# Performance work log

Measured on AMD Instinct MI355X. Metric: run time of the kernel, lower is better.

## Reference

```python
import jax, jax.numpy as jnp
import numpy as np

B, S, V, H, K, T = 4, 256, 32000, 1024, 4, 20
THRESHOLD = 0.6


def setup_inputs() -> dict:
    key = jax.random.key(0)
    ks = jax.random.split(key, 12)
    sH = 1.0 / np.sqrt(H)
    return {
        "input_ids": jax.random.randint(ks[0], (B, S), 0, V),
        "labels": jax.random.randint(ks[1], (B, S), 0, V),
        "embed": jax.random.normal(ks[2], (V, H), jnp.float32) * 0.02,
        "W1": jax.random.normal(ks[3], (H, H), jnp.float32) * sH,
        "b1": jnp.zeros((H,), jnp.float32),
        "lm_head": jax.random.normal(ks[4], (H, V), jnp.float32) * 0.02,
        "W_gen": jax.random.normal(ks[5], (H, H), jnp.float32) * sH,
        "thought_emb": jax.random.normal(ks[6], (K, H), jnp.float32) * 0.02,
        "tpos_emb": jax.random.normal(ks[7], (T, H), jnp.float32) * 0.02,
        "w_score": jax.random.normal(ks[8], (2 * H,), jnp.float32) * sH,
        "w_gate": jax.random.normal(ks[9], (2 * H,), jnp.float32) * sH,
    }


def reference(input_ids, labels, embed, W1, b1, lm_head, W_gen,
              thought_emb, tpos_emb, w_score, w_gate):
    # ---- base model: embed -> tanh MLP -> lm_head ----
    h0 = embed[input_ids]                                 # (B,S,H)
    hidden = jnp.tanh(h0 @ W1 + b1)                       # base last_hidden_state
    base_logits = hidden @ lm_head                        # (B,S,V)

    # ---- ThoughtInjector: per-position gate from normalized entropy ----
    logp = jax.nn.log_softmax(base_logits, axis=-1)
    ent = -jnp.sum(jnp.exp(logp) * logp, axis=-1) / jnp.log(float(V))  # (B,S)
    inject = (ent.mean(axis=0) > THRESHOLD) & (jnp.arange(S) < S - 1)   # (S,)

    # ---- ThoughtGenerator: (B,S,K,T,H) thoughts (masked dispatch, all pos) ----
    g = jnp.tanh(hidden @ W_gen)                          # (B,S,H)
    thoughts = jnp.tanh(g[:, :, None, None, :]
                        + thought_emb[None, None, :, None, :]
                        + tpos_emb[None, None, None, :, :])  # (B,S,K,T,H)
    tmean = thoughts.mean(axis=3)                         # (B,S,K,H) = thoughts.mean(dim=2)

    # ---- CoherenceScorer: composite score per thought ----
    comp = jax.nn.sigmoid(
        jnp.einsum('bsh,h->bs', hidden, w_score[:H])[:, :, None]
        + jnp.einsum('bskh,h->bsk', tmean, w_score[H:]))  # (B,S,K)

    # ---- MixingHead: coherence-weighted thought mix, gated blend with hidden ----
    alpha = jax.nn.softmax(comp, axis=-1)                 # (B,S,K)
    mixed_thought = jnp.einsum('bsk,bskh->bsh', alpha, tmean)
    gate = jax.nn.sigmoid(jnp.einsum('bsh,h->bs', hidden, w_gate[:H])
                          + jnp.einsum('bsh,h->bs', mixed_thought, w_gate[H:]))[..., None]
    mixed = gate * mixed_thought + (1.0 - gate) * hidden

    enhanced = jnp.where(inject[None, :, None], mixed, hidden)
    final_logits = enhanced @ lm_head                     # (B,S,V)

    # ---- shifted cross-entropy loss ----
    sl = jax.nn.log_softmax(final_logits[:, :-1, :], axis=-1)
    loss = -jnp.take_along_axis(sl, labels[:, 1:, None], axis=-1).mean()
    return final_logits, loss
```

## Files before the change

kernel.cpp:

```cpp
#include <hip/hip_runtime.h>


#define V_SZ 32000
#define H_SZ 1024
#define S_SZ 256
#define B_SZ 4
#define M_SZ 1024
#define K_TH 4
#define T_TH 20
#define NTILE_V 250
#define PARTS (NTILE_V * 2)

typedef __bf16 bf16_t;
typedef __bf16 bf16x8 __attribute__((ext_vector_type(8)));
typedef __bf16 bf16x4 __attribute__((ext_vector_type(4)));
typedef float  f32x4  __attribute__((ext_vector_type(4)));

typedef __attribute__((address_space(1))) void gvoid_t;
typedef __attribute__((address_space(3))) void lvoid_t;

__device__ __forceinline__ void async_copy16(const bf16_t* g, bf16_t* l) {
  __builtin_amdgcn_global_load_lds((gvoid_t*)g, (lvoid_t*)l, 16, 0, 0);
}

__device__ __forceinline__ float tanh_fast(float x) {
  x = fminf(fmaxf(x, -15.f), 15.f);
  float e = __expf(2.f * x);
  return (e - 1.f) / (e + 1.f);
}
__device__ __forceinline__ float sigmoid_f(float x) {
  return 1.f / (1.f + __expf(-x));
}

__device__ __forceinline__ void transpose_tile(
    const float* __restrict__ in, bf16_t* __restrict__ out, int R, int C,
    int bx, int by, float (*tile)[65], int t) {
  const int c0 = bx << 6, r0 = by << 6;
  const int tr = t >> 4, tc = (t & 15) << 2;
  #pragma unroll
  for (int i = 0; i < 4; ++i) {
    const float4 v = *(const float4*)(in + (size_t)(r0 + tr + 16 * i) * C + c0 + tc);
    tile[tr + 16 * i][tc]     = v.x;
    tile[tr + 16 * i][tc + 1] = v.y;
    tile[tr + 16 * i][tc + 2] = v.z;
    tile[tr + 16 * i][tc + 3] = v.w;
  }
  __syncthreads();
  const int wr = t >> 3, wc = (t & 7) << 3;
  #pragma unroll
  for (int i = 0; i < 2; ++i) {
    bf16x8 o;
    #pragma unroll
    for (int j = 0; j < 8; ++j) o[j] = (bf16_t)tile[wc + j][wr + 32 * i];
    *(bf16x8*)(out + (size_t)(c0 + wr + 32 * i) * R + r0 + wc) = o;
  }
}

__global__ void __launch_bounds__(256) prep_kernel(
    const float* __restrict__ lm, const float* __restrict__ W1,
    const float* __restrict__ Wg, const int* __restrict__ ids,
    const float* __restrict__ embed, bf16_t* __restrict__ lmT,
    bf16_t* __restrict__ W1T, bf16_t* __restrict__ WgT,
    bf16_t* __restrict__ X0) {
  __shared__ float tile[64][65];
  const int t = threadIdx.x;
  int bid = blockIdx.x;
  if (bid < 8000) {
    transpose_tile(lm, lmT, H_SZ, V_SZ, bid % 500, bid / 500, tile, t);
    return;
  }
  bid -= 8000;
  if (bid < 256) {
    transpose_tile(W1, W1T, H_SZ, H_SZ, bid % 16, bid / 16, tile, t);
    return;
  }
  bid -= 256;
  if (bid < 256) {
    transpose_tile(Wg, WgT, H_SZ, H_SZ, bid % 16, bid / 16, tile, t);
    return;
  }
  bid -= 256;
  const int i = bid * 256 + t;
  const int m = i >> 8, c4 = (i & 255) << 2;
  const float4 v = *(const float4*)(embed + (size_t)ids[m] * H_SZ + c4);
  bf16x4 o;
  o[0] = (bf16_t)v.x; o[1] = (bf16_t)v.y; o[2] = (bf16_t)v.z; o[3] = (bf16_t)v.w;
  *(bf16x4*)(X0 + (size_t)m * H_SZ + c4) = o;
}

template <int EPI>
__global__ void __launch_bounds__(256, 2) gemm_bt(
    const bf16_t* __restrict__ A, const bf16_t* __restrict__ BT,
    float* __restrict__ outF, bf16_t* __restrict__ outB,
    const float* __restrict__ bias, float2* __restrict__ entP,
    float* __restrict__ lseP, int mtiles, int ntiles, int N) {
  __shared__ __align__(16) bf16_t As[128 * 32];
  __shared__ __align__(16) bf16_t Bs[128 * 32];
  const int t = threadIdx.x;
  const int x = blockIdx.x & 7, y = blockIdx.x >> 3;
  const int tm = y % mtiles, tn = x + 8 * (y / mtiles);
  if (tn >= ntiles) return;
  const int m0 = tm * 128, n0 = tn * 128;
  const int lane = t & 63, wv = t >> 6, wm = wv >> 1, wn = wv & 1;
  const int col = lane & 15, qd = lane >> 4;

  const int srow = 16 * wv + (lane >> 2);
  const int schunk = ((lane & 3) ^ ((srow >> 1) & 3)) << 3;
  const bf16_t* gA0 = A  + (size_t)(m0 + srow) * 1024 + schunk;
  const bf16_t* gA1 = A  + (size_t)(m0 + srow + 64) * 1024 + schunk;
  const bf16_t* gB0 = BT + (size_t)(n0 + srow) * 1024 + schunk;
  const bf16_t* gB1 = BT + (size_t)(n0 + srow + 64) * 1024 + schunk;
  bf16_t* lA0 = As + wv * 512;
  bf16_t* lA1 = As + 2048 + wv * 512;
  bf16_t* lB0 = Bs + wv * 512;
  bf16_t* lB1 = Bs + 2048 + wv * 512;

  int offA[4], offB[4];
  #pragma unroll
  for (int i = 0; i < 4; ++i) {
    const int ra = wm * 64 + i * 16 + col;
    offA[i] = ra * 32 + ((qd ^ ((ra >> 1) & 3)) << 3);
    const int rb = wn * 64 + i * 16 + col;
    offB[i] = rb * 32 + ((qd ^ ((rb >> 1) & 3)) << 3);
  }
  f32x4 acc[4][4] = {};
  for (int kb = 0; kb < 1024; kb += 32) {
    async_copy16(gA0 + kb, lA0);
    async_copy16(gA1 + kb, lA1);
    async_copy16(gB0 + kb, lB0);
    async_copy16(gB1 + kb, lB1);
    __syncthreads();
    bf16x8 af[4], bg[4];
    #pragma unroll
    for (int mi = 0; mi < 4; ++mi) af[mi] = *(const bf16x8*)(As + offA[mi]);
    #pragma unroll
    for (int ni = 0; ni < 4; ++ni) bg[ni] = *(const bf16x8*)(Bs + offB[ni]);
    #pragma unroll
    for (int mi = 0; mi < 4; ++mi)
      #pragma unroll
      for (int ni = 0; ni < 4; ++ni)
        acc[mi][ni] = __builtin_amdgcn_mfma_f32_16x16x32_bf16(
            af[mi], bg[ni], acc[mi][ni], 0, 0, 0);
    __syncthreads();
  }

  if (EPI == 3 || EPI == 4) {
    float z[16], s[16];
    #pragma unroll
    for (int mi = 0; mi < 4; ++mi) {
      #pragma unroll
      for (int rr = 0; rr < 4; ++rr) {
        float zz = 0.f, ss = 0.f;
        #pragma unroll
        for (int ni = 0; ni < 4; ++ni) {
          const float xv = acc[mi][ni][rr];
          const float e = __expf(xv);
          zz += e;
          if (EPI == 3) ss += xv * e;
          if (EPI == 4) {
            const size_t o = (size_t)(m0 + wm * 64 + mi * 16 + qd * 4 + rr) * N
                           + (n0 + wn * 64 + ni * 16 + col);
            outF[o] = xv;
          }
        }
        z[mi * 4 + rr] = zz;
        s[mi * 4 + rr] = ss;
      }
    }
    #pragma unroll
    for (int d = 1; d < 16; d <<= 1) {
      #pragma unroll
      for (int i = 0; i < 16; ++i) {
        z[i] += __shfl_xor(z[i], d);
        if (EPI == 3) s[i] += __shfl_xor(s[i], d);
      }
    }
    if (col == 0) {
      #pragma unroll
      for (int i = 0; i < 16; ++i) {
        const int row = m0 + wm * 64 + (i >> 2) * 16 + qd * 4 + (i & 3);
        if (EPI == 3)
          entP[(size_t)row * PARTS + tn * 2 + wn] = make_float2(z[i], s[i]);
        else
          lseP[(size_t)row * PARTS + tn * 2 + wn] = z[i];
      }
    }
    return;
  }

  #pragma unroll
  for (int mi = 0; mi < 4; ++mi) {
    #pragma unroll
    for (int ni = 0; ni < 4; ++ni) {
      const int gm = m0 + wm * 64 + mi * 16 + qd * 4;
      const int gn = n0 + wn * 64 + ni * 16 + col;
      #pragma unroll
      for (int r = 0; r < 4; ++r) {
        const size_t o = (size_t)(gm + r) * N + gn;
        float v = acc[mi][ni][r];
        if (EPI == 1) {
          v = tanh_fast(v + bias[gn]);
          outF[o] = v;
          outB[o] = (bf16_t)v;
        } else if (EPI == 2) {
          outF[o] = tanh_fast(v);
        } else {
          outF[o] = v;
        }
      }
    }
  }
}

__global__ void __launch_bounds__(256) lse_merge_kernel(
    const float* __restrict__ lseP, float* __restrict__ lse) {
  const int t = threadIdx.x, w = t >> 6, lane = t & 63;
  const int row = blockIdx.x * 4 + w;
  float z = 0.f;
  for (int i = lane; i < PARTS; i += 64) z += lseP[(size_t)row * PARTS + i];
  #pragma unroll
  for (int d = 1; d < 64; d <<= 1) z += __shfl_xor(z, d);
  if (lane == 0) lse[row] = __logf(z);
}

__device__ __forceinline__ float block_sum(float v, float* red, int t) {
  red[t] = v;
  __syncthreads();
  for (int off = 128; off > 0; off >>= 1) {
    if (t < off) red[t] += red[t + off];
    __syncthreads();
  }
  const float r = red[0];
  __syncthreads();
  return r;
}

__global__ void __launch_bounds__(256) mix_kernel(
    const float* __restrict__ hidden, const float* __restrict__ gF,
    const float* __restrict__ th_emb, const float* __restrict__ tpos,
    const float* __restrict__ w_score, const float* __restrict__ w_gate,
    const float2* __restrict__ entP, bf16_t* __restrict__ enhB) {
  const int m = blockIdx.x, t = threadIdx.x, s = m & (S_SZ - 1);
  __shared__ float red[256];
  __shared__ float se[4];

  {
    const int w = t >> 6, lane = t & 63;
    const int row = w * S_SZ + s;
    float z = 0.f, sv = 0.f;
    for (int i = lane; i < PARTS; i += 64) {
      const float2 pz = entP[(size_t)row * PARTS + i];
      z += pz.x; sv += pz.y;
    }
    #pragma unroll
    for (int d = 1; d < 64; d <<= 1) {
      z += __shfl_xor(z, d);
      sv += __shfl_xor(sv, d);
    }
    if (lane == 0) se[w] = __logf(z) - sv / z;
    __syncthreads();
  }
  const float emean = 0.25f * (se[0] + se[1] + se[2] + se[3]);
  const int inj = (emean * (1.0f / 10.373491f) > 0.6f) && (s < S_SZ - 1);

  float hv[4], ws1[4], ws2[4], wg1[4], wg2[4], tmv[4][4];
  #pragma unroll
  for (int j = 0; j < 4; ++j) {
    const int h = t + 256 * j;
    hv[j]  = hidden[(size_t)m * H_SZ + h];
    ws1[j] = w_score[h];      ws2[j] = w_score[H_SZ + h];
    wg1[j] = w_gate[h];       wg2[j] = w_gate[H_SZ + h];
    const float gv = gF[(size_t)m * H_SZ + h];
    float tp[T_TH];
    #pragma unroll
    for (int tt = 0; tt < T_TH; ++tt) tp[tt] = tpos[tt * H_SZ + h];
    #pragma unroll
    for (int k = 0; k < 4; ++k) {
      const float base = gv + th_emb[k * H_SZ + h];
      float ssum = 0.f;
      #pragma unroll
      for (int tt = 0; tt < T_TH; ++tt) ssum += tanh_fast(base + tp[tt]);
      tmv[k][j] = ssum * (1.f / T_TH);
    }
  }
  float ph = 0.f, pg = 0.f;
  #pragma unroll
  for (int j = 0; j < 4; ++j) { ph += hv[j] * ws1[j]; pg += hv[j] * wg1[j]; }
  const float sh = block_sum(ph, red, t);
  const float gh = block_sum(pg, red, t);
  float comp[4];
  #pragma unroll
  for (int k = 0; k < 4; ++k) {
    float pc = 0.f;
    #pragma unroll
    for (int j = 0; j < 4; ++j) pc += tmv[k][j] * ws2[j];
    const float ck = block_sum(pc, red, t);
    comp[k] = sigmoid_f(sh + ck);
  }
  const float ma = fmaxf(fmaxf(comp[0], comp[1]), fmaxf(comp[2], comp[3]));
  float al[4], asum = 0.f;
  #pragma unroll
  for (int k = 0; k < 4; ++k) { al[k] = __expf(comp[k] - ma); asum += al[k]; }
  const float inv = 1.f / asum;
  float mx[4];
  #pragma unroll
  for (int j = 0; j < 4; ++j) {
    mx[j] = 0.f;
    #pragma unroll
    for (int k = 0; k < 4; ++k) mx[j] += al[k] * inv * tmv[k][j];
  }
  float pm = 0.f;
  #pragma unroll
  for (int j = 0; j < 4; ++j) pm += mx[j] * wg2[j];
  const float gm = block_sum(pm, red, t);
  const float gate = sigmoid_f(gh + gm);
  #pragma unroll
  for (int j = 0; j < 4; ++j) {
    const float e = inj ? (gate * mx[j] + (1.f - gate) * hv[j]) : hv[j];
    enhB[(size_t)m * H_SZ + t + 256 * j] = (bf16_t)e;
  }
}

__global__ void __launch_bounds__(256) loss_kernel(
    const float* __restrict__ logits, const float* __restrict__ lse,
    const int* __restrict__ labels, float* __restrict__ out_loss) {
  const int t = threadIdx.x;
  float acc = 0.f;
  for (int i = t; i < (S_SZ - 1) * B_SZ; i += 256) {
    const int b = i / (S_SZ - 1), s2 = i % (S_SZ - 1);
    const int m = b * S_SZ + s2;
    const int lab = labels[m + 1];
    acc += lse[m] - logits[(size_t)m * V_SZ + lab];
  }
  __shared__ float red[256];
  red[t] = acc;
  __syncthreads();
  for (int off = 128; off > 0; off >>= 1) {
    if (t < off) red[t] += red[t + off];
    __syncthreads();
  }
  if (t == 0) out_loss[0] = red[0] / (float)((S_SZ - 1) * B_SZ);
}

extern "C" void kernel_launch(void* const* d_in, const int* in_sizes, int n_in,
                              void* d_out, int out_size, void* d_ws, size_t ws_size,
                              hipStream_t stream) {
  const int*   ids    = (const int*)  d_in[0];
  const int*   labels = (const int*)  d_in[1];
  const float* embed  = (const float*)d_in[2];
  const float* W1     = (const float*)d_in[3];
  const float* b1     = (const float*)d_in[4];
  const float* lm     = (const float*)d_in[5];
  const float* Wg     = (const float*)d_in[6];
  const float* thE    = (const float*)d_in[7];
  const float* tpos   = (const float*)d_in[8];
  const float* wsc    = (const float*)d_in[9];
  const float* wgt    = (const float*)d_in[10];
  float* out = (float*)d_out;

  char* p = (char*)d_ws;
  auto carve = [&p](size_t bytes) {
    char* r = p;
    p += (bytes + 255) & ~(size_t)255;
    return r;
  };
  bf16_t* lmT   = (bf16_t*)carve((size_t)V_SZ * H_SZ * sizeof(bf16_t));
  bf16_t* W1T   = (bf16_t*)carve((size_t)H_SZ * H_SZ * sizeof(bf16_t));
  bf16_t* WgT   = (bf16_t*)carve((size_t)H_SZ * H_SZ * sizeof(bf16_t));
  bf16_t* X0    = (bf16_t*)carve((size_t)M_SZ * H_SZ * sizeof(bf16_t));
  bf16_t* hidB  = (bf16_t*)carve((size_t)M_SZ * H_SZ * sizeof(bf16_t));
  bf16_t* enhB  = (bf16_t*)carve((size_t)M_SZ * H_SZ * sizeof(bf16_t));
  float*  hidF  = (float*) carve((size_t)M_SZ * H_SZ * sizeof(float));
  float*  gF    = (float*) carve((size_t)M_SZ * H_SZ * sizeof(float));
  float*  partials = (float*)carve((size_t)M_SZ * PARTS * sizeof(float2));
  float*  lse   = (float*) carve(M_SZ * sizeof(float));
  float2* entP = (float2*)partials;
  float*  lseP = (float*)partials;

  prep_kernel<<<9536, 256, 0, stream>>>(lm, W1, Wg, ids, embed, lmT, W1T, WgT, X0);

  gemm_bt<1><<<64, 256, 0, stream>>>(X0, W1T, hidF, hidB, b1, nullptr, nullptr, 8, 8, H_SZ);
  gemm_bt<2><<<64, 256, 0, stream>>>(hidB, WgT, gF, nullptr, nullptr, nullptr, nullptr, 8, 8, H_SZ);
  gemm_bt<3><<<2048, 256, 0, stream>>>(hidB, lmT, nullptr, nullptr, nullptr, entP, nullptr, 8, NTILE_V, V_SZ);

  mix_kernel<<<M_SZ, 256, 0, stream>>>(hidF, gF, thE, tpos, wsc, wgt, entP, enhB);

  gemm_bt<4><<<2048, 256, 0, stream>>>(enhB, lmT, out, nullptr, nullptr, nullptr, lseP, 8, NTILE_V, V_SZ);
  lse_merge_kernel<<<M_SZ / 4, 256, 0, stream>>>(lseP, lse);
  loss_kernel<<<1, 256, 0, stream>>>(out, lse, labels, out + (size_t)M_SZ * V_SZ);
}
```

Before: 596.5 us.

## Add 256x256 triple-buffered vocab GEMM kernel with split MFMA phases

Replaces the 128x128 single-buffered GEMM used for both vocab-sized projections with a new 512-thread kernel that computes 256x256 tiles. Shared memory is triple-buffered, loads are issued two k-steps ahead, waits use explicit vmcnt, and wave priority is raised around the MFMA batches. The aim is to overlap global loads with matrix math and to cut lm_head reloads by using larger tiles. The cost is much higher register and LDS use, which may lower occupancy. There are now fewer blocks (512) for about 256 CUs, which risks uneven load across the tail.

```diff
diff --git a/kernel.cpp b/kernel.cpp
--- a/kernel.cpp
+++ b/kernel.cpp
@@ -8,8 +8,8 @@
 #define M_SZ 1024
 #define K_TH 4
 #define T_TH 20
-#define NTILE_V 250
-#define PARTS (NTILE_V * 2)
+#define NTILE_V 125
+#define PARTS (NTILE_V * 4)
 
 typedef __bf16 bf16_t;
 typedef __bf16 bf16x8 __attribute__((ext_vector_type(8)));
@@ -92,8 +92,7 @@
 __global__ void __launch_bounds__(256, 2) gemm_bt(
     const bf16_t* __restrict__ A, const bf16_t* __restrict__ BT,
     float* __restrict__ outF, bf16_t* __restrict__ outB,
-    const float* __restrict__ bias, float2* __restrict__ entP,
-    float* __restrict__ lseP, int mtiles, int ntiles, int N) {
+    const float* __restrict__ bias, int mtiles, int ntiles, int N) {
   __shared__ __align__(16) bf16_t As[128 * 32];
   __shared__ __align__(16) bf16_t Bs[128 * 32];
   const int t = threadIdx.x;
@@ -143,51 +142,6 @@
             af[mi], bg[ni], acc[mi][ni], 0, 0, 0);
     __syncthreads();
   }
-
-  if (EPI == 3 || EPI == 4) {
-    float z[16], s[16];
-    #pragma unroll
-    for (int mi = 0; mi < 4; ++mi) {
-      #pragma unroll
-      for (int rr = 0; rr < 4; ++rr) {
-        float zz = 0.f, ss = 0.f;
-        #pragma unroll
-        for (int ni = 0; ni < 4; ++ni) {
-          const float xv = acc[mi][ni][rr];
-          const float e = __expf(xv);
-          zz += e;
-          if (EPI == 3) ss += xv * e;
-          if (EPI == 4) {
-            const size_t o = (size_t)(m0 + wm * 64 + mi * 16 + qd * 4 + rr) * N
-                           + (n0 + wn * 64 + ni * 16 + col);
-            outF[o] = xv;
-          }
-        }
-        z[mi * 4 + rr] = zz;
-        s[mi * 4 + rr] = ss;
-      }
-    }
-    #pragma unroll
-    for (int d = 1; d < 16; d <<= 1) {
-      #pragma unroll
-      for (int i = 0; i < 16; ++i) {
-        z[i] += __shfl_xor(z[i], d);
-        if (EPI == 3) s[i] += __shfl_xor(s[i], d);
-      }
-    }
-    if (col == 0) {
-      #pragma unroll
-      for (int i = 0; i < 16; ++i) {
-        const int row = m0 + wm * 64 + (i >> 2) * 16 + qd * 4 + (i & 3);
-        if (EPI == 3)
-          entP[(size_t)row * PARTS + tn * 2 + wn] = make_float2(z[i], s[i]);
-        else
-          lseP[(size_t)row * PARTS + tn * 2 + wn] = z[i];
-      }
-    }
-    return;
-  }
-
   #pragma unroll
   for (int mi = 0; mi < 4; ++mi) {
     #pragma unroll
@@ -202,11 +156,140 @@
           v = tanh_fast(v + bias[gn]);
           outF[o] = v;
           outB[o] = (bf16_t)v;
-        } else if (EPI == 2) {
+        } else {
           outF[o] = tanh_fast(v);
-        } else {
-          outF[o] = v;
         }
+      }
+    }
+  }
+}
+
+template <int EPI>
+__global__ void __launch_bounds__(512, 2) gemm_big(
+    const bf16_t* __restrict__ A, const bf16_t* __restrict__ BT,
+    float* __restrict__ outF, float2* __restrict__ entP,
+    float* __restrict__ lseP, int mtiles, int ntiles, int N) {
+  __shared__ __align__(16) bf16_t As[3][256 * 32];
+  __shared__ __align__(16) bf16_t Bs[3][256 * 32];
+  const int t = threadIdx.x;
+  const int x = blockIdx.x & 7, y = blockIdx.x >> 3;
+  const int tm = y % mtiles, tn = x + 8 * (y / mtiles);
+  if (tn >= ntiles) return;
+  const int m0 = tm * 256, n0 = tn * 256;
+  const int lane = t & 63, wv = t >> 6;
+  const int wm = wv >> 2, wn = wv & 3;
+  const int col = lane & 15, qd = lane >> 4;
+
+  int ldsOff[2], srow[2], sch[2];
+  #pragma unroll
+  for (int j = 0; j < 2; ++j) {
+    const int cid = j * 512 + wv * 64 + lane;
+    srow[j] = cid >> 2;
+    sch[j] = ((cid & 3) ^ ((srow[j] >> 1) & 3)) << 3;
+    ldsOff[j] = (j * 512 + wv * 64) * 8;
+  }
+  const bf16_t* gA0 = A  + (size_t)(m0 + srow[0]) * 1024 + sch[0];
+  const bf16_t* gA1 = A  + (size_t)(m0 + srow[1]) * 1024 + sch[1];
+  const bf16_t* gB0 = BT + (size_t)(n0 + srow[0]) * 1024 + sch[0];
+  const bf16_t* gB1 = BT + (size_t)(n0 + srow[1]) * 1024 + sch[1];
+
+  int offA[8], offB[4];
+  #pragma unroll
+  for (int i = 0; i < 8; ++i) {
+    const int ra = wm * 128 + i * 16 + col;
+    offA[i] = ra * 32 + ((qd ^ ((ra >> 1) & 3)) << 3);
+  }
+  #pragma unroll
+  for (int i = 0; i < 4; ++i) {
+    const int rb = wn * 64 + i * 16 + col;
+    offB[i] = rb * 32 + ((qd ^ ((rb >> 1) & 3)) << 3);
+  }
+
+  f32x4 acc[8][4] = {};
+
+  async_copy16(gA0, &As[0][ldsOff[0]]);
+  async_copy16(gA1, &As[0][ldsOff[1]]);
+  async_copy16(gB0, &Bs[0][ldsOff[0]]);
+  async_copy16(gB1, &Bs[0][ldsOff[1]]);
+  async_copy16(gA0 + 32, &As[1][ldsOff[0]]);
+  async_copy16(gA1 + 32, &As[1][ldsOff[1]]);
+  async_copy16(gB0 + 32, &Bs[1][ldsOff[0]]);
+  async_copy16(gB1 + 32, &Bs[1][ldsOff[1]]);
+  asm volatile("s_waitcnt vmcnt(4)" ::: "memory");
+  __builtin_amdgcn_sched_barrier(0);
+  __builtin_amdgcn_s_barrier();
+
+  int cur = 0;
+  for (int kt = 0; kt < 32; ++kt) {
+    const bf16_t* __restrict__ Ab = &As[cur][0];
+    const bf16_t* __restrict__ Bb = &Bs[cur][0];
+    const int nb = (cur == 0) ? 2 : cur - 1;
+    const int kb2 = (kt + 2) * 32;
+    bf16x8 af[8], b0, b1;
+    #pragma unroll
+    for (int i = 0; i < 8; ++i) af[i] = *(const bf16x8*)(Ab + offA[i]);
+    b0 = *(const bf16x8*)(Bb + offB[0]);
+    b1 = *(const bf16x8*)(Bb + offB[1]);
+    if (kt < 30) {
+      async_copy16(gA0 + kb2, &As[nb][ldsOff[0]]);
+      async_copy16(gA1 + kb2, &As[nb][ldsOff[1]]);
+    }
+    __builtin_amdgcn_s_barrier();
+    __builtin_amdgcn_s_setprio(1);
+    #pragma unroll
+    for (int i = 0; i < 8; ++i) {
+      acc[i][0] = __builtin_amdgcn_mfma_f32_16x16x32_bf16(af[i], b0, acc[i][0], 0, 0, 0);
+      acc[i][1] = __builtin_amdgcn_mfma_f32_16x16x32_bf16(af[i], b1, acc[i][1], 0, 0, 0);
+    }
+    __builtin_amdgcn_s_setprio(0);
+    __builtin_amdgcn_s_barrier();
+    b0 = *(const bf16x8*)(Bb + offB[2]);
+    b1 = *(const bf16x8*)(Bb + offB[3]);
+    if (kt < 30) {
+      async_copy16(gB0 + kb2, &Bs[nb][ldsOff[0]]);
+      async_copy16(gB1 + kb2, &Bs[nb][ldsOff[1]]);
+      asm volatile("s_waitcnt vmcnt(4)" ::: "memory");
+    } else if (kt == 30) {
+      asm volatile("s_waitcnt vmcnt(0)" ::: "memory");
+    }
+    __builtin_amdgcn_sched_barrier(0);
+    __builtin_amdgcn_s_barrier();
+    __builtin_amdgcn_s_setprio(1);
+    #pragma unroll
+    for (int i = 0; i < 8; ++i) {
+      acc[i][2] = __builtin_amdgcn_mfma_f32_16x16x32_bf16(af[i], b0, acc[i][2], 0, 0, 0);
+      acc[i][3] = __builtin_amdgcn_mfma_f32_16x16x32_bf16(af[i], b1, acc[i][3], 0, 0, 0);
+    }
+    __builtin_amdgcn_s_setprio(0);
+    __builtin_amdgcn_s_barrier();
+    cur = (cur == 2) ? 0 : cur + 1;
+  }
+
+  #pragma unroll
+  for (int mi = 0; mi < 8; ++mi) {
+    #pragma unroll
+    for (int rr = 0; rr < 4; ++rr) {
+      const int row = m0 + wm * 128 + mi * 16 + qd * 4 + rr;
+      float zz = 0.f, ss = 0.f;
+      #pragma unroll
+      for (int ni = 0; ni < 4; ++ni) {
+        const float xv = acc[mi][ni][rr];
+        const float e = __expf(xv);
+        zz += e;
+        if (EPI == 3) ss += xv * e;
+        if (EPI == 4)
+          outF[(size_t)row * N + n0 + wn * 64 + ni * 16 + col] = xv;
+      }
+      #pragma unroll
+      for (int d = 1; d < 16; d <<= 1) {
+        zz += __shfl_xor(zz, d);
+        if (EPI == 3) ss += __shfl_xor(ss, d);
+      }
+      if (col == 0) {
+        if (EPI == 3)
+          entP[(size_t)row * PARTS + tn * 4 + wn] = make_float2(zz, ss);
+        else
+          lseP[(size_t)row * PARTS + tn * 4 + wn] = zz;
       }
     }
   }
@@ -379,13 +462,13 @@
 
   prep_kernel<<<9536, 256, 0, stream>>>(lm, W1, Wg, ids, embed, lmT, W1T, WgT, X0);
 
-  gemm_bt<1><<<64, 256, 0, stream>>>(X0, W1T, hidF, hidB, b1, nullptr, nullptr, 8, 8, H_SZ);
-  gemm_bt<2><<<64, 256, 0, stream>>>(hidB, WgT, gF, nullptr, nullptr, nullptr, nullptr, 8, 8, H_SZ);
-  gemm_bt<3><<<2048, 256, 0, stream>>>(hidB, lmT, nullptr, nullptr, nullptr, entP, nullptr, 8, NTILE_V, V_SZ);
+  gemm_bt<1><<<64, 256, 0, stream>>>(X0, W1T, hidF, hidB, b1, 8, 8, H_SZ);
+  gemm_bt<2><<<64, 256, 0, stream>>>(hidB, WgT, gF, nullptr, nullptr, 8, 8, H_SZ);
+  gemm_big<3><<<512, 512, 0, stream>>>(hidB, lmT, nullptr, entP, nullptr, 4, NTILE_V, V_SZ);
 
   mix_kernel<<<M_SZ, 256, 0, stream>>>(hidF, gF, thE, tpos, wsc, wgt, entP, enhB);
 
-  gemm_bt<4><<<2048, 256, 0, stream>>>(enhB, lmT, out, nullptr, nullptr, nullptr, lseP, 8, NTILE_V, V_SZ);
+  gemm_big<4><<<512, 512, 0, stream>>>(enhB, lmT, out, nullptr, lseP, 4, NTILE_V, V_SZ);
   lse_merge_kernel<<<M_SZ / 4, 256, 0, stream>>>(lseP, lse);
   loss_kernel<<<1, 256, 0, stream>>>(out, lse, labels, out + (size_t)M_SZ * V_SZ);
 }
```

New measurement: 588.2 us. Within noise of the previous version (-1.4%).
